# Performance work log

Measured on AMD Instinct MI355X. Metric: run time of the kernel, lower is better.

## Reference

```python
import jax, jax.numpy as jnp
import numpy as np

N_NODES = 100000
N_EDGES = 1600000
N_GRAPHS = 512
IN_DIM = 128
HID = 128
EDGE_DIM = 16
BN_EPS = 1e-5


def _gine_conv(x, edge_index, edge_attr, le_w, le_b, W1, b1, gamma, beta, W2, b2):
    # GINEConv (eps=0): out = MLP(x + sum_j ReLU(x_j + Lin(edge_attr_j)))
    src, dst = edge_index[0], edge_index[1]
    e = edge_attr @ le_w + le_b                      # [E, F]
    msg = jax.nn.relu(x[src] + e)                    # gather + add + relu
    agg = jax.ops.segment_sum(msg, dst, num_segments=N_NODES)
    h = agg + x                                      # (1+eps)*x, eps=0
    h = h @ W1 + b1
    mean = jnp.mean(h, axis=0)
    var = jnp.var(h, axis=0)
    h = (h - mean) * jax.lax.rsqrt(var + BN_EPS) * gamma + beta  # BatchNorm1d (batch stats)
    h = jax.nn.relu(h)
    return h @ W2 + b2


def setup_inputs() -> dict:
    key = jax.random.key(0)
    ks = jax.random.split(key, 20)
    s = 0.02
    inp = {
        'x': jax.random.normal(ks[0], (N_NODES, IN_DIM), jnp.float32),
        'edge_index': jax.random.randint(ks[1], (2, N_EDGES), 0, N_NODES, jnp.int32),
        'edge_attr': jax.random.normal(ks[2], (N_EDGES, EDGE_DIM), jnp.float32),
        'batch': jnp.sort(jax.random.randint(ks[3], (N_NODES,), 0, N_GRAPHS, jnp.int32)),
        # conv1 params
        'le1_w': jax.random.normal(ks[4], (EDGE_DIM, IN_DIM), jnp.float32) * s,
        'le1_b': jnp.zeros((IN_DIM,), jnp.float32),
        'W11': jax.random.normal(ks[5], (IN_DIM, HID), jnp.float32) * s,
        'b11': jnp.zeros((HID,), jnp.float32),
        'g1': jnp.ones((HID,), jnp.float32),
        'bt1': jnp.zeros((HID,), jnp.float32),
        'W12': jax.random.normal(ks[6], (HID, HID), jnp.float32) * s,
        'b12': jnp.zeros((HID,), jnp.float32),
        # conv2 params
        'le2_w': jax.random.normal(ks[7], (EDGE_DIM, HID), jnp.float32) * s,
        'le2_b': jnp.zeros((HID,), jnp.float32),
        'W21': jax.random.normal(ks[8], (HID, HID), jnp.float32) * s,
        'b21': jnp.zeros((HID,), jnp.float32),
        'g2': jnp.ones((HID,), jnp.float32),
        'bt2': jnp.zeros((HID,), jnp.float32),
        'W22': jax.random.normal(ks[9], (HID, HID), jnp.float32) * s,
        'b22': jnp.zeros((HID,), jnp.float32),
        # classifier
        'Wc1': jax.random.normal(ks[10], (HID, 64), jnp.float32) * s,
        'bc1': jnp.zeros((64,), jnp.float32),
        'Wc2': jax.random.normal(ks[11], (64, 2), jnp.float32) * s,
        'bc2': jnp.zeros((2,), jnp.float32),
    }
    return inp


def reference(x, edge_index, edge_attr, batch,
              le1_w, le1_b, W11, b11, g1, bt1, W12, b12,
              le2_w, le2_b, W21, b21, g2, bt2, W22, b22,
              Wc1, bc1, Wc2, bc2):
    h = jax.nn.relu(_gine_conv(x, edge_index, edge_attr, le1_w, le1_b, W11, b11, g1, bt1, W12, b12))
    h = jax.nn.relu(_gine_conv(h, edge_index, edge_attr, le2_w, le2_b, W21, b21, g2, bt2, W22, b22))
    pooled = jax.ops.segment_sum(h, batch, num_segments=N_GRAPHS)  # global_add_pool
    h = jax.nn.relu(pooled @ Wc1 + bc1)
    # Dropout(0.5) treated as identity (eval-mode reference)
    return h @ Wc2 + bc2
```

## Files before the change

### kernel.cpp

```cpp
#include <hip/hip_runtime.h>
#include <hip/hip_fp16.h>

#define N_NODES  100000
#define N_EDGES  1600000
#define N_GRAPHS 512
#define DIM      128
#define EDGE_DIM 16
#define BN_EPS   1e-5f


__global__ __launch_bounds__(256) void k_hist(const int* __restrict__ dst,
                                              int* __restrict__ deg) {
    int e = blockIdx.x * 256 + threadIdx.x;
    if (e < N_EDGES) atomicAdd(&deg[dst[e]], 1);
}

__global__ __launch_bounds__(256) void k_scan1(const int* __restrict__ deg,
                                               int* __restrict__ rowptr1,
                                               int* __restrict__ sums, int N) {
    __shared__ int sc[256];
    int t = threadIdx.x;
    int base = blockIdx.x * 1024 + t * 4;
    int v0 = (base + 0 < N) ? deg[base + 0] : 0;
    int v1 = (base + 1 < N) ? deg[base + 1] : 0;
    int v2 = (base + 2 < N) ? deg[base + 2] : 0;
    int v3 = (base + 3 < N) ? deg[base + 3] : 0;
    v1 += v0; v2 += v1; v3 += v2;
    sc[t] = v3;
    __syncthreads();
    for (int o = 1; o < 256; o <<= 1) {
        int add = (t >= o) ? sc[t - o] : 0;
        __syncthreads();
        sc[t] += add;
        __syncthreads();
    }
    int prefix = sc[t] - v3;
    if (base + 0 < N) rowptr1[base + 0] = v0 + prefix;
    if (base + 1 < N) rowptr1[base + 1] = v1 + prefix;
    if (base + 2 < N) rowptr1[base + 2] = v2 + prefix;
    if (base + 3 < N) rowptr1[base + 3] = v3 + prefix;
    if (t == 255) sums[blockIdx.x] = sc[255];
}

__global__ __launch_bounds__(256) void k_scan2(int* __restrict__ sums, int n) {
    __shared__ int sc[256];
    int t = threadIdx.x;
    int v = (t < n) ? sums[t] : 0;
    sc[t] = v;
    __syncthreads();
    for (int o = 1; o < 256; o <<= 1) {
        int add = (t >= o) ? sc[t - o] : 0;
        __syncthreads();
        sc[t] += add;
        __syncthreads();
    }
    if (t < n) sums[t] = sc[t];
}

__global__ __launch_bounds__(256) void k_scan3(int* __restrict__ rowptr,
                                               int* __restrict__ cursor,
                                               const int* __restrict__ sums, int N) {
    int c = blockIdx.x;
    int off = (c == 0) ? 0 : sums[c - 1];
    int t = threadIdx.x;
    int base = c * 1024 + t * 4;
#pragma unroll
    for (int i = 0; i < 4; i++) {
        int g = base + i;
        if (g < N) {
            int val = rowptr[1 + g] + off;
            rowptr[1 + g] = val;
            if (g + 1 < N) cursor[g + 1] = val;
        }
    }
    if (c == 0 && t == 0) { rowptr[0] = 0; cursor[0] = 0; }
}

__global__ __launch_bounds__(256) void k_fill(const int* __restrict__ src,
                                              const int* __restrict__ dst,
                                              const float* __restrict__ edge_attr,
                                              int* __restrict__ cursor,
                                              int* __restrict__ csr_src,
                                              uint4* __restrict__ csr_ea) {
    int e = blockIdx.x * 256 + threadIdx.x;
    if (e < N_EDGES) {
        int d = dst[e];
        int p = atomicAdd(&cursor[d], 1);
        csr_src[p] = src[e];
        const float4* ea = (const float4*)(edge_attr + (size_t)e * EDGE_DIM);
        float4 a0 = ea[0], a1 = ea[1], a2 = ea[2], a3 = ea[3];
        union { __half h[16]; uint4 q[2]; } u;
        u.h[0]  = __float2half(a0.x); u.h[1]  = __float2half(a0.y);
        u.h[2]  = __float2half(a0.z); u.h[3]  = __float2half(a0.w);
        u.h[4]  = __float2half(a1.x); u.h[5]  = __float2half(a1.y);
        u.h[6]  = __float2half(a1.z); u.h[7]  = __float2half(a1.w);
        u.h[8]  = __float2half(a2.x); u.h[9]  = __float2half(a2.y);
        u.h[10] = __float2half(a2.z); u.h[11] = __float2half(a2.w);
        u.h[12] = __float2half(a3.x); u.h[13] = __float2half(a3.y);
        u.h[14] = __float2half(a3.z); u.h[15] = __float2half(a3.w);
        uint4* o = csr_ea + (size_t)p * 2;
        o[0] = u.q[0]; o[1] = u.q[1];
    }
}

__device__ __forceinline__ void edge_acc(float2 xr, uint4 q0, uint4 q1,
                                         const float* wl0, const float* wl1,
                                         float b0, float b1,
                                         float& acc0, float& acc1) {
    union { uint4 q[2]; __half h[16]; } u;
    u.q[0] = q0; u.q[1] = q1;
    float e0 = b0, e1 = b1;
#pragma unroll
    for (int k = 0; k < 16; k++) {
        float a = __half2float(u.h[k]);
        e0 = fmaf(a, wl0[k], e0);
        e1 = fmaf(a, wl1[k], e1);
    }
    acc0 += fmaxf(xr.x + e0, 0.f);
    acc1 += fmaxf(xr.y + e1, 0.f);
}

__global__ __launch_bounds__(256) void k_gine_msg(const float* __restrict__ x,
                                                  const uint4* __restrict__ csr_ea,
                                                  const int* __restrict__ rowptr,
                                                  const int* __restrict__ csr_src,
                                                  const float* __restrict__ lew,
                                                  const float* __restrict__ leb,
                                                  float* __restrict__ agg) {
    int lane = threadIdx.x & 63;
    int node = blockIdx.x * 4 + (threadIdx.x >> 6);
    int f0 = lane * 2;

    float wl0[EDGE_DIM], wl1[EDGE_DIM];
#pragma unroll
    for (int k = 0; k < EDGE_DIM; k++) {
        wl0[k] = lew[k * DIM + f0];
        wl1[k] = lew[k * DIM + f0 + 1];
    }
    float b0 = leb[f0], b1 = leb[f0 + 1];

    float2 xv = *(const float2*)(x + (size_t)node * DIM + f0);
    float acc0 = xv.x, acc1 = xv.y;

    int pbeg = __builtin_amdgcn_readfirstlane(rowptr[node]);
    int pend = __builtin_amdgcn_readfirstlane(rowptr[node + 1]);

    int p = pbeg;
    for (; p + 4 <= pend; p += 4) {
        int s0 = __builtin_amdgcn_readfirstlane(csr_src[p + 0]);
        int s1 = __builtin_amdgcn_readfirstlane(csr_src[p + 1]);
        int s2 = __builtin_amdgcn_readfirstlane(csr_src[p + 2]);
        int s3 = __builtin_amdgcn_readfirstlane(csr_src[p + 3]);

        const uint4* ea = csr_ea + (size_t)p * 2;
        uint4 a00 = ea[0], a01 = ea[1];
        uint4 a10 = ea[2], a11 = ea[3];
        uint4 a20 = ea[4], a21 = ea[5];
        uint4 a30 = ea[6], a31 = ea[7];

        float2 x0 = *(const float2*)(x + (size_t)s0 * DIM + f0);
        float2 x1 = *(const float2*)(x + (size_t)s1 * DIM + f0);
        float2 x2 = *(const float2*)(x + (size_t)s2 * DIM + f0);
        float2 x3 = *(const float2*)(x + (size_t)s3 * DIM + f0);

        edge_acc(x0, a00, a01, wl0, wl1, b0, b1, acc0, acc1);
        edge_acc(x1, a10, a11, wl0, wl1, b0, b1, acc0, acc1);
        edge_acc(x2, a20, a21, wl0, wl1, b0, b1, acc0, acc1);
        edge_acc(x3, a30, a31, wl0, wl1, b0, b1, acc0, acc1);
    }
    for (; p < pend; p++) {
        int s0 = __builtin_amdgcn_readfirstlane(csr_src[p]);
        const uint4* ea = csr_ea + (size_t)p * 2;
        uint4 a0 = ea[0], a1 = ea[1];
        float2 x0 = *(const float2*)(x + (size_t)s0 * DIM + f0);
        edge_acc(x0, a0, a1, wl0, wl1, b0, b1, acc0, acc1);
    }

    float2 o; o.x = acc0; o.y = acc1;
    *(float2*)(agg + (size_t)node * DIM + f0) = o;
}

template <int MODE>
__global__ __launch_bounds__(256) void k_gemm(const float* __restrict__ A,
                                              const float* __restrict__ W,
                                              const float* __restrict__ bias,
                                              const float* __restrict__ coef,
                                              float* __restrict__ out, int M) {
    __shared__ float As[32][DIM];
    int t = threadIdx.x;
    int rbase = blockIdx.x * 32;

#pragma unroll
    for (int i = 0; i < 16; i++) {
        int idx = t + i * 256;
        int r = idx >> 7, c = idx & 127;
        int gr = rbase + r;
        float v = (gr < M) ? A[(size_t)gr * DIM + c] : 0.f;
        if (MODE == 1) {
            v = coef[c] * v + coef[DIM + c];
            v = v > 0.f ? v : 0.f;
        }
        As[r][c] = v;
    }
    __syncthreads();

    int cq = (t & 31) * 4;
    int rg = (t >> 5) * 4;
    float acc[4][4] = {{0.f}};

    for (int k = 0; k < DIM; k++) {
        float4 w = *(const float4*)&W[(size_t)k * DIM + cq];
        float a0 = As[rg + 0][k], a1 = As[rg + 1][k];
        float a2 = As[rg + 2][k], a3 = As[rg + 3][k];
        acc[0][0] += a0 * w.x; acc[0][1] += a0 * w.y; acc[0][2] += a0 * w.z; acc[0][3] += a0 * w.w;
        acc[1][0] += a1 * w.x; acc[1][1] += a1 * w.y; acc[1][2] += a1 * w.z; acc[1][3] += a1 * w.w;
        acc[2][0] += a2 * w.x; acc[2][1] += a2 * w.y; acc[2][2] += a2 * w.z; acc[2][3] += a2 * w.w;
        acc[3][0] += a3 * w.x; acc[3][1] += a3 * w.y; acc[3][2] += a3 * w.z; acc[3][3] += a3 * w.w;
    }

    float4 bb = *(const float4*)&bias[cq];
#pragma unroll
    for (int i = 0; i < 4; i++) {
        int gr = rbase + rg + i;
        if (gr < M) {
            float4 o;
            o.x = acc[i][0] + bb.x;
            o.y = acc[i][1] + bb.y;
            o.z = acc[i][2] + bb.z;
            o.w = acc[i][3] + bb.w;
            if (MODE == 1) {
                o.x = o.x > 0.f ? o.x : 0.f;
                o.y = o.y > 0.f ? o.y : 0.f;
                o.z = o.z > 0.f ? o.z : 0.f;
                o.w = o.w > 0.f ? o.w : 0.f;
            }
            *(float4*)&out[(size_t)gr * DIM + cq] = o;
        }
    }
}

__global__ __launch_bounds__(512) void k_colstats(const float* __restrict__ h,
                                                  float* __restrict__ colstat, int M) {
    __shared__ float redS[4][DIM];
    __shared__ float redQ[4][DIM];
    int c = threadIdx.x & 127;
    int rg = threadIdx.x >> 7;
    float s = 0.f, ss = 0.f;
    for (int r = blockIdx.x * 4 + rg; r < M; r += gridDim.x * 4) {
        float v = h[(size_t)r * DIM + c];
        s += v;
        ss += v * v;
    }
    redS[rg][c] = s; redQ[rg][c] = ss;
    __syncthreads();
    if (rg == 0) {
        s  = redS[0][c] + redS[1][c] + redS[2][c] + redS[3][c];
        ss = redQ[0][c] + redQ[1][c] + redQ[2][c] + redQ[3][c];
        atomicAdd(&colstat[c], s);
        atomicAdd(&colstat[DIM + c], ss);
    }
}

__global__ __launch_bounds__(128) void k_bncoef(const float* __restrict__ colstat,
                                                const float* __restrict__ gamma,
                                                const float* __restrict__ beta,
                                                float* __restrict__ coef) {
    int c = threadIdx.x;
    float inv_n = 1.f / (float)N_NODES;
    float mean = colstat[c] * inv_n;
    float var = colstat[DIM + c] * inv_n - mean * mean;
    float a = gamma[c] * rsqrtf(var + BN_EPS);
    coef[c] = a;
    coef[DIM + c] = beta[c] - mean * a;
}

__global__ __launch_bounds__(256) void k_pool(const float* __restrict__ h,
                                              const int* __restrict__ batch,
                                              float* __restrict__ pooled) {
    __shared__ float red[DIM];
    int g = blockIdx.x;
    int c = threadIdx.x & 127;
    int rg = threadIdx.x >> 7;
    int lo = 0, hi = N_NODES;
    while (lo < hi) { int mid = (lo + hi) >> 1; if (batch[mid] < g) lo = mid + 1; else hi = mid; }
    int start = lo;
    hi = N_NODES;
    while (lo < hi) { int mid = (lo + hi) >> 1; if (batch[mid] < g + 1) lo = mid + 1; else hi = mid; }
    int end = lo;
    float s = 0.f;
    for (int n = start + rg; n < end; n += 2) s += h[(size_t)n * DIM + c];
    if (rg == 1) red[c] = s;
    __syncthreads();
    if (rg == 0) pooled[g * DIM + c] = s + red[c];
}

__global__ __launch_bounds__(64) void k_cls(const float* __restrict__ pooled,
                                            const float* __restrict__ Wc1,
                                            const float* __restrict__ bc1,
                                            const float* __restrict__ Wc2,
                                            const float* __restrict__ bc2,
                                            float* __restrict__ out) {
    __shared__ float row[DIM];
    __shared__ float t1[64];
    int g = blockIdx.x, t = threadIdx.x;
    row[t] = pooled[g * DIM + t];
    row[64 + t] = pooled[g * DIM + 64 + t];
    __syncthreads();
    float acc = bc1[t];
    for (int k = 0; k < DIM; k++) acc += row[k] * Wc1[k * 64 + t];
    t1[t] = acc > 0.f ? acc : 0.f;
    __syncthreads();
    if (t < 2) {
        float o = bc2[t];
        for (int j = 0; j < 64; j++) o += t1[j] * Wc2[j * 2 + t];
        out[g * 2 + t] = o;
    }
}


extern "C" void kernel_launch(void* const* d_in, const int* in_sizes, int n_in,
                              void* d_out, int out_size, void* d_ws, size_t ws_size,
                              hipStream_t stream) {
    const float* x          = (const float*)d_in[0];
    const int*   edge_index = (const int*)d_in[1];
    const float* edge_attr  = (const float*)d_in[2];
    const int*   batch      = (const int*)d_in[3];
    const float* le1_w = (const float*)d_in[4];
    const float* le1_b = (const float*)d_in[5];
    const float* W11   = (const float*)d_in[6];
    const float* b11   = (const float*)d_in[7];
    const float* g1    = (const float*)d_in[8];
    const float* bt1   = (const float*)d_in[9];
    const float* W12   = (const float*)d_in[10];
    const float* b12   = (const float*)d_in[11];
    const float* le2_w = (const float*)d_in[12];
    const float* le2_b = (const float*)d_in[13];
    const float* W21   = (const float*)d_in[14];
    const float* b21   = (const float*)d_in[15];
    const float* g2    = (const float*)d_in[16];
    const float* bt2   = (const float*)d_in[17];
    const float* W22   = (const float*)d_in[18];
    const float* b22   = (const float*)d_in[19];
    const float* Wc1   = (const float*)d_in[20];
    const float* bc1   = (const float*)d_in[21];
    const float* Wc2   = (const float*)d_in[22];
    const float* bc2   = (const float*)d_in[23];
    float* out = (float*)d_out;

    const int* srcp = edge_index;
    const int* dstp = edge_index + N_EDGES;

    char* ws = (char*)d_ws;
    size_t off = 0;
    auto carve = [&](size_t bytes) -> char* {
        char* p = ws + off;
        off += (bytes + 255) & ~(size_t)255;
        return p;
    };
    float* X0      = (float*)carve((size_t)N_NODES * DIM * 4);
    float* X1      = (float*)carve((size_t)N_NODES * DIM * 4);
    int*   rowptr  = (int*)carve((size_t)(N_NODES + 1) * 4);
    int*   cursor  = (int*)carve((size_t)N_NODES * 4);
    int*   sums    = (int*)carve(256 * 4);
    int*   csr_src = (int*)carve((size_t)N_EDGES * 4);
    uint4* csr_ea  = (uint4*)carve((size_t)N_EDGES * 32);
    float* colstat = (float*)carve(2 * DIM * 4);
    float* coef    = (float*)carve(2 * DIM * 4);
    float* pooled  = (float*)carve((size_t)N_GRAPHS * DIM * 4);
    (void)ws_size; (void)in_sizes; (void)n_in; (void)out_size;

    const int nch = (N_NODES + 1023) / 1024;

    hipMemsetAsync(cursor, 0, (size_t)N_NODES * 4, stream);
    k_hist<<<(N_EDGES + 255) / 256, 256, 0, stream>>>(dstp, cursor);
    k_scan1<<<nch, 256, 0, stream>>>(cursor, rowptr + 1, sums, N_NODES);
    k_scan2<<<1, 256, 0, stream>>>(sums, nch);
    k_scan3<<<nch, 256, 0, stream>>>(rowptr, cursor, sums, N_NODES);
    k_fill<<<(N_EDGES + 255) / 256, 256, 0, stream>>>(srcp, dstp, edge_attr, cursor,
                                                      csr_src, csr_ea);

    k_gine_msg<<<N_NODES / 4, 256, 0, stream>>>(x, csr_ea, rowptr, csr_src, le1_w, le1_b, X0);
    k_gemm<0><<<(N_NODES + 31) / 32, 256, 0, stream>>>(X0, W11, b11, nullptr, X1, N_NODES);
    hipMemsetAsync(colstat, 0, 2 * DIM * 4, stream);
    k_colstats<<<256, 512, 0, stream>>>(X1, colstat, N_NODES);
    k_bncoef<<<1, 128, 0, stream>>>(colstat, g1, bt1, coef);
    k_gemm<1><<<(N_NODES + 31) / 32, 256, 0, stream>>>(X1, W12, b12, coef, X0, N_NODES);

    k_gine_msg<<<N_NODES / 4, 256, 0, stream>>>(X0, csr_ea, rowptr, csr_src, le2_w, le2_b, X1);
    k_gemm<0><<<(N_NODES + 31) / 32, 256, 0, stream>>>(X1, W21, b21, nullptr, X0, N_NODES);
    hipMemsetAsync(colstat, 0, 2 * DIM * 4, stream);
    k_colstats<<<256, 512, 0, stream>>>(X0, colstat, N_NODES);
    k_bncoef<<<1, 128, 0, stream>>>(colstat, g2, bt2, coef);
    k_gemm<1><<<(N_NODES + 31) / 32, 256, 0, stream>>>(X0, W22, b22, coef, X1, N_NODES);

    k_pool<<<N_GRAPHS, 256, 0, stream>>>(X1, batch, pooled);
    k_cls<<<N_GRAPHS, 64, 0, stream>>>(pooled, Wc1, bc1, Wc2, bc2, out);
}
```

Measured before the change: 979.2 us.

## Fuse BN stats, coef, and pooling into GEMM epilogues; use fdot2 for edge linear

Column sum and sum-of-squares for BatchNorm are now accumulated in the first GEMM's epilogue, and the BN coefficients are computed in the prologue of the second GEMM. This removes the separate colstats and bncoef kernels and one full re-read of the hidden matrix. The final GEMM atomically accumulates into pooled graph sums instead of writing its output and running a separate pool kernel. The edge-linear inner loop now uses packed half dot products with fp16 weights, which lowers precision of the edge-weight term and adds atomic contention on the pooled and colstat buffers.

```diff
diff --git a/kernel.cpp b/kernel.cpp
--- a/kernel.cpp
+++ b/kernel.cpp
@@ -7,6 +7,14 @@
 #define DIM      128
 #define EDGE_DIM 16
 #define BN_EPS   1e-5f
+
+typedef _Float16 h2 __attribute__((ext_vector_type(2)));
+
+#if defined(__has_builtin)
+#if __has_builtin(__builtin_amdgcn_fdot2)
+#define HAVE_FDOT2 1
+#endif
+#endif
 
 
 __global__ __launch_bounds__(256) void k_hist(const int* __restrict__ dst,
@@ -103,19 +111,28 @@
     }
 }
 
+union EaU { uint4 q[2]; h2 p[8]; };
+
 __device__ __forceinline__ void edge_acc(float2 xr, uint4 q0, uint4 q1,
-                                         const float* wl0, const float* wl1,
+                                         const h2* wl0p, const h2* wl1p,
                                          float b0, float b1,
                                          float& acc0, float& acc1) {
-    union { uint4 q[2]; __half h[16]; } u;
-    u.q[0] = q0; u.q[1] = q1;
+    EaU u; u.q[0] = q0; u.q[1] = q1;
     float e0 = b0, e1 = b1;
-#pragma unroll
-    for (int k = 0; k < 16; k++) {
-        float a = __half2float(u.h[k]);
-        e0 = fmaf(a, wl0[k], e0);
-        e1 = fmaf(a, wl1[k], e1);
-    }
+#if HAVE_FDOT2
+#pragma unroll
+    for (int j = 0; j < 8; j++) {
+        e0 = __builtin_amdgcn_fdot2(u.p[j], wl0p[j], e0, false);
+        e1 = __builtin_amdgcn_fdot2(u.p[j], wl1p[j], e1, false);
+    }
+#else
+#pragma unroll
+    for (int j = 0; j < 8; j++) {
+        float ax = (float)u.p[j].x, ay = (float)u.p[j].y;
+        e0 = fmaf(ax, (float)wl0p[j].x, fmaf(ay, (float)wl0p[j].y, e0));
+        e1 = fmaf(ax, (float)wl1p[j].x, fmaf(ay, (float)wl1p[j].y, e1));
+    }
+#endif
     acc0 += fmaxf(xr.x + e0, 0.f);
     acc1 += fmaxf(xr.y + e1, 0.f);
 }
@@ -131,11 +148,15 @@
     int node = blockIdx.x * 4 + (threadIdx.x >> 6);
     int f0 = lane * 2;
 
-    float wl0[EDGE_DIM], wl1[EDGE_DIM];
-#pragma unroll
-    for (int k = 0; k < EDGE_DIM; k++) {
-        wl0[k] = lew[k * DIM + f0];
-        wl1[k] = lew[k * DIM + f0 + 1];
+    h2 wl0p[8], wl1p[8];
+#pragma unroll
+    for (int j = 0; j < 8; j++) {
+        h2 a, b;
+        a.x = (_Float16)lew[(2 * j + 0) * DIM + f0];
+        a.y = (_Float16)lew[(2 * j + 1) * DIM + f0];
+        b.x = (_Float16)lew[(2 * j + 0) * DIM + f0 + 1];
+        b.y = (_Float16)lew[(2 * j + 1) * DIM + f0 + 1];
+        wl0p[j] = a; wl1p[j] = b;
     }
     float b0 = leb[f0], b1 = leb[f0 + 1];
 
@@ -163,17 +184,17 @@
         float2 x2 = *(const float2*)(x + (size_t)s2 * DIM + f0);
         float2 x3 = *(const float2*)(x + (size_t)s3 * DIM + f0);
 
-        edge_acc(x0, a00, a01, wl0, wl1, b0, b1, acc0, acc1);
-        edge_acc(x1, a10, a11, wl0, wl1, b0, b1, acc0, acc1);
-        edge_acc(x2, a20, a21, wl0, wl1, b0, b1, acc0, acc1);
-        edge_acc(x3, a30, a31, wl0, wl1, b0, b1, acc0, acc1);
+        edge_acc(x0, a00, a01, wl0p, wl1p, b0, b1, acc0, acc1);
+        edge_acc(x1, a10, a11, wl0p, wl1p, b0, b1, acc0, acc1);
+        edge_acc(x2, a20, a21, wl0p, wl1p, b0, b1, acc0, acc1);
+        edge_acc(x3, a30, a31, wl0p, wl1p, b0, b1, acc0, acc1);
     }
     for (; p < pend; p++) {
         int s0 = __builtin_amdgcn_readfirstlane(csr_src[p]);
         const uint4* ea = csr_ea + (size_t)p * 2;
         uint4 a0 = ea[0], a1 = ea[1];
         float2 x0 = *(const float2*)(x + (size_t)s0 * DIM + f0);
-        edge_acc(x0, a0, a1, wl0, wl1, b0, b1, acc0, acc1);
+        edge_acc(x0, a0, a1, wl0p, wl1p, b0, b1, acc0, acc1);
     }
 
     float2 o; o.x = acc0; o.y = acc1;
@@ -184,11 +205,28 @@
 __global__ __launch_bounds__(256) void k_gemm(const float* __restrict__ A,
                                               const float* __restrict__ W,
                                               const float* __restrict__ bias,
-                                              const float* __restrict__ coef,
+                                              float* __restrict__ colstat,
+                                              const float* __restrict__ gamma,
+                                              const float* __restrict__ beta,
+                                              const int* __restrict__ batch,
+                                              float* __restrict__ pooled,
                                               float* __restrict__ out, int M) {
     __shared__ float As[32][DIM];
+    __shared__ float cA[DIM], cB[DIM];
     int t = threadIdx.x;
     int rbase = blockIdx.x * 32;
+
+    if (MODE != 0) {
+        if (t < DIM) {
+            float inv_n = 1.f / (float)N_NODES;
+            float mean = colstat[t] * inv_n;
+            float var = colstat[DIM + t] * inv_n - mean * mean;
+            float a = gamma[t] * rsqrtf(var + BN_EPS);
+            cA[t] = a;
+            cB[t] = beta[t] - mean * a;
+        }
+        __syncthreads();
+    }
 
 #pragma unroll
     for (int i = 0; i < 16; i++) {
@@ -196,8 +234,8 @@
         int r = idx >> 7, c = idx & 127;
         int gr = rbase + r;
         float v = (gr < M) ? A[(size_t)gr * DIM + c] : 0.f;
-        if (MODE == 1) {
-            v = coef[c] * v + coef[DIM + c];
+        if (MODE != 0) {
+            v = cA[c] * v + cB[c];
             v = v > 0.f ? v : 0.f;
         }
         As[r][c] = v;
@@ -219,79 +257,92 @@
     }
 
     float4 bb = *(const float4*)&bias[cq];
+    float o[4][4];
 #pragma unroll
     for (int i = 0; i < 4; i++) {
-        int gr = rbase + rg + i;
-        if (gr < M) {
-            float4 o;
-            o.x = acc[i][0] + bb.x;
-            o.y = acc[i][1] + bb.y;
-            o.z = acc[i][2] + bb.z;
-            o.w = acc[i][3] + bb.w;
-            if (MODE == 1) {
-                o.x = o.x > 0.f ? o.x : 0.f;
-                o.y = o.y > 0.f ? o.y : 0.f;
-                o.z = o.z > 0.f ? o.z : 0.f;
-                o.w = o.w > 0.f ? o.w : 0.f;
+        o[i][0] = acc[i][0] + bb.x;
+        o[i][1] = acc[i][1] + bb.y;
+        o[i][2] = acc[i][2] + bb.z;
+        o[i][3] = acc[i][3] + bb.w;
+        if (MODE != 0) {
+#pragma unroll
+            for (int j = 0; j < 4; j++) o[i][j] = o[i][j] > 0.f ? o[i][j] : 0.f;
+        }
+    }
+
+    if (MODE != 2) {
+#pragma unroll
+        for (int i = 0; i < 4; i++) {
+            int gr = rbase + rg + i;
+            if (gr < M) {
+                float4 v; v.x = o[i][0]; v.y = o[i][1]; v.z = o[i][2]; v.w = o[i][3];
+                *(float4*)&out[(size_t)gr * DIM + cq] = v;
             }
-            *(float4*)&out[(size_t)gr * DIM + cq] = o;
-        }
-    }
-}
-
-__global__ __launch_bounds__(512) void k_colstats(const float* __restrict__ h,
-                                                  float* __restrict__ colstat, int M) {
-    __shared__ float redS[4][DIM];
-    __shared__ float redQ[4][DIM];
-    int c = threadIdx.x & 127;
-    int rg = threadIdx.x >> 7;
-    float s = 0.f, ss = 0.f;
-    for (int r = blockIdx.x * 4 + rg; r < M; r += gridDim.x * 4) {
-        float v = h[(size_t)r * DIM + c];
-        s += v;
-        ss += v * v;
-    }
-    redS[rg][c] = s; redQ[rg][c] = ss;
-    __syncthreads();
-    if (rg == 0) {
-        s  = redS[0][c] + redS[1][c] + redS[2][c] + redS[3][c];
-        ss = redQ[0][c] + redQ[1][c] + redQ[2][c] + redQ[3][c];
-        atomicAdd(&colstat[c], s);
-        atomicAdd(&colstat[DIM + c], ss);
-    }
-}
-
-__global__ __launch_bounds__(128) void k_bncoef(const float* __restrict__ colstat,
-                                                const float* __restrict__ gamma,
-                                                const float* __restrict__ beta,
-                                                float* __restrict__ coef) {
-    int c = threadIdx.x;
-    float inv_n = 1.f / (float)N_NODES;
-    float mean = colstat[c] * inv_n;
-    float var = colstat[DIM + c] * inv_n - mean * mean;
-    float a = gamma[c] * rsqrtf(var + BN_EPS);
-    coef[c] = a;
-    coef[DIM + c] = beta[c] - mean * a;
-}
-
-__global__ __launch_bounds__(256) void k_pool(const float* __restrict__ h,
-                                              const int* __restrict__ batch,
-                                              float* __restrict__ pooled) {
-    __shared__ float red[DIM];
-    int g = blockIdx.x;
-    int c = threadIdx.x & 127;
-    int rg = threadIdx.x >> 7;
-    int lo = 0, hi = N_NODES;
-    while (lo < hi) { int mid = (lo + hi) >> 1; if (batch[mid] < g) lo = mid + 1; else hi = mid; }
-    int start = lo;
-    hi = N_NODES;
-    while (lo < hi) { int mid = (lo + hi) >> 1; if (batch[mid] < g + 1) lo = mid + 1; else hi = mid; }
-    int end = lo;
-    float s = 0.f;
-    for (int n = start + rg; n < end; n += 2) s += h[(size_t)n * DIM + c];
-    if (rg == 1) red[c] = s;
-    __syncthreads();
-    if (rg == 0) pooled[g * DIM + c] = s + red[c];
+        }
+    }
+
+    if (MODE == 0) {
+        float s[4] = {0.f, 0.f, 0.f, 0.f}, q[4] = {0.f, 0.f, 0.f, 0.f};
+#pragma unroll
+        for (int i = 0; i < 4; i++) {
+            int gr = rbase + rg + i;
+            if (gr < M) {
+#pragma unroll
+                for (int j = 0; j < 4; j++) {
+                    s[j] += o[i][j];
+                    q[j] += o[i][j] * o[i][j];
+                }
+            }
+        }
+        __syncthreads();
+        float* s1 = &As[0][0];
+        float* s2 = &As[8][0];
+        int rgi = t >> 5;
+#pragma unroll
+        for (int j = 0; j < 4; j++) {
+            s1[rgi * DIM + cq + j] = s[j];
+            s2[rgi * DIM + cq + j] = q[j];
+        }
+        __syncthreads();
+        if (rgi == 0) {
+#pragma unroll
+            for (int j = 0; j < 4; j++) {
+                float ts = 0.f, tq = 0.f;
+#pragma unroll
+                for (int k = 0; k < 8; k++) {
+                    ts += s1[k * DIM + cq + j];
+                    tq += s2[k * DIM + cq + j];
+                }
+                atomicAdd(&colstat[cq + j], ts);
+                atomicAdd(&colstat[DIM + cq + j], tq);
+            }
+        }
+    }
+
+    if (MODE == 2) {
+        int gr0 = rbase + rg;
+        int b0 = (gr0 + 0 < M) ? batch[gr0 + 0] : -1;
+        int b1 = (gr0 + 1 < M) ? batch[gr0 + 1] : -1;
+        int b2 = (gr0 + 2 < M) ? batch[gr0 + 2] : -1;
+        int b3 = (gr0 + 3 < M) ? batch[gr0 + 3] : -1;
+        if (b0 == b3 && b0 >= 0) {
+#pragma unroll
+            for (int j = 0; j < 4; j++) {
+                float v = o[0][j] + o[1][j] + o[2][j] + o[3][j];
+                atomicAdd(&pooled[(size_t)b0 * DIM + cq + j], v);
+            }
+        } else {
+            int bs[4] = {b0, b1, b2, b3};
+#pragma unroll
+            for (int i = 0; i < 4; i++) {
+                if (bs[i] >= 0) {
+#pragma unroll
+                    for (int j = 0; j < 4; j++)
+                        atomicAdd(&pooled[(size_t)bs[i] * DIM + cq + j], o[i][j]);
+                }
+            }
+        }
+    }
 }
 
 __global__ __launch_bounds__(64) void k_cls(const float* __restrict__ pooled,
@@ -364,14 +415,18 @@
     int*   sums    = (int*)carve(256 * 4);
     int*   csr_src = (int*)carve((size_t)N_EDGES * 4);
     uint4* csr_ea  = (uint4*)carve((size_t)N_EDGES * 32);
-    float* colstat = (float*)carve(2 * DIM * 4);
-    float* coef    = (float*)carve(2 * DIM * 4);
-    float* pooled  = (float*)carve((size_t)N_GRAPHS * DIM * 4);
+    float* zreg    = (float*)carve((2 * DIM + 2 * DIM + (size_t)N_GRAPHS * DIM) * 4);
+    float* colstat1 = zreg;
+    float* colstat2 = zreg + 2 * DIM;
+    float* pooled   = zreg + 4 * DIM;
     (void)ws_size; (void)in_sizes; (void)n_in; (void)out_size;
 
     const int nch = (N_NODES + 1023) / 1024;
+    const int ngb = (N_NODES + 31) / 32;
 
     hipMemsetAsync(cursor, 0, (size_t)N_NODES * 4, stream);
+    hipMemsetAsync(zreg, 0, (4 * DIM + (size_t)N_GRAPHS * DIM) * 4, stream);
+
     k_hist<<<(N_EDGES + 255) / 256, 256, 0, stream>>>(dstp, cursor);
     k_scan1<<<nch, 256, 0, stream>>>(cursor, rowptr + 1, sums, N_NODES);
     k_scan2<<<1, 256, 0, stream>>>(sums, nch);
@@ -380,19 +435,16 @@
                                                       csr_src, csr_ea);
 
     k_gine_msg<<<N_NODES / 4, 256, 0, stream>>>(x, csr_ea, rowptr, csr_src, le1_w, le1_b, X0);
-    k_gemm<0><<<(N_NODES + 31) / 32, 256, 0, stream>>>(X0, W11, b11, nullptr, X1, N_NODES);
-    hipMemsetAsync(colstat, 0, 2 * DIM * 4, stream);
-    k_colstats<<<256, 512, 0, stream>>>(X1, colstat, N_NODES);
-    k_bncoef<<<1, 128, 0, stream>>>(colstat, g1, bt1, coef);
-    k_gemm<1><<<(N_NODES + 31) / 32, 256, 0, stream>>>(X1, W12, b12, coef, X0, N_NODES);
+    k_gemm<0><<<ngb, 256, 0, stream>>>(X0, W11, b11, colstat1, nullptr, nullptr,
+                                       nullptr, nullptr, X1, N_NODES);
+    k_gemm<1><<<ngb, 256, 0, stream>>>(X1, W12, b12, colstat1, g1, bt1,
+                                       nullptr, nullptr, X0, N_NODES);
 
     k_gine_msg<<<N_NODES / 4, 256, 0, stream>>>(X0, csr_ea, rowptr, csr_src, le2_w, le2_b, X1);
-    k_gemm<0><<<(N_NODES + 31) / 32, 256, 0, stream>>>(X1, W21, b21, nullptr, X0, N_NODES);
-    hipMemsetAsync(colstat, 0, 2 * DIM * 4, stream);
-    k_colstats<<<256, 512, 0, stream>>>(X0, colstat, N_NODES);
-    k_bncoef<<<1, 128, 0, stream>>>(colstat, g2, bt2, coef);
-    k_gemm<1><<<(N_NODES + 31) / 32, 256, 0, stream>>>(X0, W22, b22, coef, X1, N_NODES);
-
-    k_pool<<<N_GRAPHS, 256, 0, stream>>>(X1, batch, pooled);
+    k_gemm<0><<<ngb, 256, 0, stream>>>(X1, W21, b21, colstat2, nullptr, nullptr,
+                                       nullptr, nullptr, X0, N_NODES);
+    k_gemm<2><<<ngb, 256, 0, stream>>>(X0, W22, b22, colstat2, g2, bt2,
+                                       batch, pooled, nullptr, N_NODES);
+
     k_cls<<<N_GRAPHS, 64, 0, stream>>>(pooled, Wc1, bc1, Wc2, bc2, out);
 }
```

After: 1.446 ms. 1.48x slower.
